# Kernel optimization log

Hardware: AMD Instinct MI355X
Metric: run time of the kernel (lower is better)

Reference implementation:

```python
import jax, jax.numpy as jnp
from jax import lax
import numpy as np


def _normalize(x):
    # F.normalize(dim=-1), eps=1e-12
    return x / jnp.clip(jnp.linalg.norm(x, axis=-1, keepdims=True), 1e-12, None)


def _masked_log_softmax(logits, mask):
    # softmax restricted to active columns (emulates gathering active objects)
    return jax.nn.log_softmax(jnp.where(mask, logits, -1e9), axis=-1)


def _aabb_iou(gc, gs, pc, ps):
    # gc,gs: (B,L,3) gt center/size; pc,ps: (B,P,3) pred center/size -> iou (B,L,P)
    # create_box_batch builds axis-aligned corner boxes, so box3d_overlap == AABB IoU
    gmin = (gc - gs * 0.5)[:, :, None, :]
    gmax = (gc + gs * 0.5)[:, :, None, :]
    pmin = (pc - ps * 0.5)[:, None, :, :]
    pmax = (pc + ps * 0.5)[:, None, :, :]
    inter = jnp.prod(jnp.clip(jnp.minimum(gmax, pmax) - jnp.maximum(gmin, pmin), 0.0, None), axis=-1)
    vol_g = jnp.prod(gs, axis=-1)[:, :, None]
    vol_p = jnp.prod(ps, axis=-1)[:, None, :]
    return inter / (vol_g + vol_p - inter + 1e-7)


def setup_inputs() -> dict:
    key = jax.random.key(0)
    ks = jax.random.split(key, 11)
    B, P, L, H = 32, 1024, 32, 128
    return {
        'pred_center': jax.random.normal(ks[0], (B, P, 3), jnp.float32),
        'pred_size': jax.random.uniform(ks[1], (B, P, 3), jnp.float32, 0.2, 1.5),
        'bbox_feature': jax.random.normal(ks[2], (B, P, H), jnp.float32),
        'gt_center': jax.random.normal(ks[3], (B, L, 3), jnp.float32),
        'gt_size': jax.random.uniform(ks[4], (B, L, 3), jnp.float32, 0.2, 1.5),
        'lang_emb': jax.random.normal(ks[5], (B * L, H), jnp.float32),
        'objectness_scores': jax.random.normal(ks[6], (B, P, 2), jnp.float32),
        'Wt': jax.random.normal(ks[7], (H, H), jnp.float32) * (1.0 / np.sqrt(H)),
        'Wp': jax.random.normal(ks[8], (H, H), jnp.float32) * (1.0 / np.sqrt(H)),
        'Wpi': jax.random.normal(ks[9], (H, H), jnp.float32) * (1.0 / np.sqrt(H)),
        'lang_num': jax.random.randint(ks[10], (B,), 1, L + 1, jnp.int64),
    }


def reference(pred_center, pred_size, bbox_feature, gt_center, gt_size,
              lang_emb, objectness_scores, Wt, Wp, Wpi, lang_num):
    sg = lax.stop_gradient
    B, P = pred_center.shape[:2]
    L = gt_center.shape[1]

    # objectness mask (argmax over 2 classes), detached
    obj_mask = (jnp.argmax(objectness_scores, axis=-1) == 1).astype(jnp.float32)  # (B,P)
    cmask = obj_mask > 0
    cnt = obj_mask.sum(-1)                       # active objects per sample
    cnt1 = jnp.maximum(cnt, 1.0)

    # 3D IoU between gt boxes (size + 0.01, as in forward) and predicted boxes; all detached
    iou = _aabb_iou(sg(gt_center), sg(gt_size) + 0.01, sg(pred_center), sg(pred_size))  # (B,L,P)
    tgt = (iou > 0.25).astype(jnp.float32) * obj_mask[:, None, :]  # (B,L,P), detached

    # ---- language-box contrastive (NCE) ----
    text = _normalize(jnp.einsum('bld,hd->blh', lang_emb.reshape(B, L, -1), Wt))   # (B,L,H)
    boxl = _normalize(jnp.einsum('bpd,hd->bph', bbox_feature, Wp))                 # (B,P,H)
    sim_lang = jnp.einsum('blh,bph->blp', text, boxl)                              # (B,L,P)
    ls = _masked_log_softmax(sim_lang, cmask[:, None, :])
    loss_v = (-ls * tgt).sum(-1) / cnt1[:, None]                                   # mean over cnt cols
    # transposed logits are (cnt,1): log_softmax over a single logit is 0 -> loss_t == 0
    lang_nce = 0.5 * loss_v                                                        # (B,L)

    lang_active = (jnp.arange(L)[None, :] < lang_num[:, None]).astype(jnp.float32)
    lang_con_loss = (lang_nce * lang_active).sum() / B

    # ---- box-box contrastive (NCE) ----
    boxi = _normalize(jnp.einsum('bpd,hd->bph', bbox_feature, Wpi))                # (B,P,H)
    sim_iou = jnp.einsum('bph,bqh->bpq', boxi, boxi)                               # (B,P,P)
    ls_r = _masked_log_softmax(sim_iou, cmask[:, None, :])
    ls_c = _masked_log_softmax(jnp.swapaxes(sim_iou, 1, 2), cmask[:, None, :])
    # target(b,l,p,q) = tgt(b,l,p)*tgt(b,l,q); contract without materializing (B,L,P,P)
    lv = jnp.einsum('blp,bpq,blq->bl', tgt, -ls_r, tgt) / (cnt1 ** 2)[:, None]
    lt = jnp.einsum('blp,bpq,blq->bl', tgt, -ls_c, tgt) / (cnt1 ** 2)[:, None]
    iou_nce = 0.5 * (lv + lt)                                                      # (B,L)
    iou_con_loss = (iou_nce * lang_active).sum() / B

    return jnp.stack([lang_con_loss, iou_con_loss])
```

## Files before the change

kernel.cpp:

```cpp
#include <hip/hip_runtime.h>
#include <hip/hip_bf16.h>
#include <math.h>

typedef unsigned short u16;
typedef unsigned int   u32;
typedef unsigned char  u8;
typedef unsigned long long u64;

typedef __attribute__((ext_vector_type(8))) short short8_t;
typedef __attribute__((ext_vector_type(4))) float f32x4_t;

#define H128 128

__device__ __forceinline__ float bf2f(u16 v){
    u32 u = ((u32)v) << 16;
    return __uint_as_float(u);
}
__device__ __forceinline__ u16 f2bf(float x){
    u32 u = __float_as_uint(x);
    u32 r = (u + 0x7fffu + ((u >> 16) & 1u)) >> 16;
    return (u16)r;
}
__device__ __forceinline__ void unpack8(uint4 v, float* f){
    f[0] = bf2f((u16)(v.x & 0xffff)); f[1] = bf2f((u16)(v.x >> 16));
    f[2] = bf2f((u16)(v.y & 0xffff)); f[3] = bf2f((u16)(v.y >> 16));
    f[4] = bf2f((u16)(v.z & 0xffff)); f[5] = bf2f((u16)(v.z >> 16));
    f[6] = bf2f((u16)(v.w & 0xffff)); f[7] = bf2f((u16)(v.w >> 16));
}
__device__ __forceinline__ float ld1(const void* p, size_t i, int F){
    return F ? ((const float*)p)[i] : bf2f(((const u16*)p)[i]);
}
__device__ __forceinline__ void ld8(const void* p, size_t i, int F, float* f){
    if (F){
        const float* fp = (const float*)p + i;
        float4 a = *(const float4*)fp;
        float4 b = *(const float4*)(fp + 4);
        f[0]=a.x; f[1]=a.y; f[2]=a.z; f[3]=a.w;
        f[4]=b.x; f[5]=b.y; f[6]=b.z; f[7]=b.w;
    } else {
        uint4 v = *(const uint4*)((const u16*)p + i);
        unpack8(v, f);
    }
}
__device__ __forceinline__ float clampf(float x, float lo, float hi){
    return fminf(fmaxf(x, lo), hi);
}
__device__ __forceinline__ int detectF(const void* pred_size, int* Fs){
    int tid = threadIdx.x;
    if (tid < 64){
        const u16* ps = (const u16*)pred_size;
        u16 v0 = ps[tid], v1 = ps[tid + 64];
        int cc = ((v0 >= 0x3000 && v0 < 0x4100) ? 1 : 0)
               + ((v1 >= 0x3000 && v1 < 0x4100) ? 1 : 0);
        #pragma unroll
        for (int off = 32; off > 0; off >>= 1) cc += __shfl_xor(cc, off);
        if (tid == 0) *Fs = (cc >= 120) ? 0 : 1;
    }
    __syncthreads();
    return *Fs;
}

__device__ void prep_fn(char* smem,
        const void* obj, const void* gtc, const void* gts,
        const void* pc_, const void* ps_, int F,
        u8* mask, float* cnt_part, u8* tgt, float* tcnt_part,
        int* needcnt_part, int* needlist, int* acnt_part, int* alist,
        int b0, int P, int L, int bblk)
{
    int tid = threadIdx.x;
    int ntile = P / 256;
    int b = bblk / ntile, ct = bblk % ntile;
    int p = ct * 256 + tid;

    float* gtb = (float*)smem;
    float* tl  = gtb + (size_t)L * 8;
    float* red = tl + L;
    int*   wb  = (int*)(red + 256);
    int*   wb2 = wb + 4;

    if (tid < L){
        float gmn[3], gmx[3], gss[3];
        for (int i = 0; i < 3; i++){
            size_t gi = ((size_t)(b0 + b) * L + tid) * 3 + i;
            float gc  = ld1(gtc, gi, F);
            float gsv = ld1(gts, gi, F) + 0.01f;
            gmn[i] = gc - 0.5f * gsv; gmx[i] = gc + 0.5f * gsv; gss[i] = gsv;
        }
        float* r = &gtb[tid * 8];
        r[0] = gmn[0]; r[1] = gmn[1]; r[2] = gmn[2];
        r[3] = gmx[0]; r[4] = gmx[1]; r[5] = gmx[2];
        r[6] = gss[0] * gss[1] * gss[2];
        tl[tid] = 0.f;
    }
    __syncthreads();

    size_t ob = ((size_t)(b0 + b) * P + p) * 2;
    float s0 = ld1(obj, ob, F), s1 = ld1(obj, ob + 1, F);
    u8 m = (s1 > s0) ? 1 : 0;
    mask[(size_t)b * P + p] = m;

    size_t pb = ((size_t)(b0 + b) * P + p) * 3;
    float pl[3], ph[3], volp = 1.f;
    for (int i = 0; i < 3; i++){
        float pcv = ld1(pc_, pb + i, F), psv = ld1(ps_, pb + i, F);
        pl[i] = pcv - 0.5f * psv; ph[i] = pcv + 0.5f * psv; volp *= psv;
    }
    bool any = false;
    for (int l = 0; l < L; l++){
        float* r = &gtb[l * 8];
        float inter = 1.f;
        for (int i = 0; i < 3; i++){
            float mn = fmaxf(r[i],     pl[i]);
            float mx = fminf(r[3 + i], ph[i]);
            inter *= fmaxf(mx - mn, 0.f);
        }
        float iou = inter / (r[6] + volp - inter + 1e-7f);
        u8 t = (iou > 0.25f && m) ? 1 : 0;
        tgt[((size_t)b * L + l) * P + p] = t;
        if (t){ any = true; atomicAdd(&tl[l], 1.f); }
    }

    int wid = tid >> 6, lane = tid & 63;
    u64 bal  = __ballot(any);
    u64 bal2 = __ballot(m != 0);
    if (lane == 0){ wb[wid] = __popcll(bal); wb2[wid] = __popcll(bal2); }
    red[tid] = (float)m;
    __syncthreads();
    if (tid == 0){
        int s = 0;
        for (int w = 0; w < 4; w++){ int cn = wb[w];  wb[w]  = s; s += cn; }
        needcnt_part[b * 4 + ct] = s;
        s = 0;
        for (int w = 0; w < 4; w++){ int cn = wb2[w]; wb2[w] = s; s += cn; }
        acnt_part[b * 4 + ct] = s;
    }
    __syncthreads();
    if (any){
        int rank = __popcll(bal & ((1ULL << lane) - 1ULL));
        needlist[(size_t)b * P + ct * 256 + wb[wid] + rank] = p;
    }
    if (m){
        int rank = __popcll(bal2 & ((1ULL << lane) - 1ULL));
        alist[(size_t)b * P + ct * 256 + wb2[wid] + rank] = p;
    }
    for (int st = 128; st > 0; st >>= 1){
        if (tid < st) red[tid] += red[tid + st];
        __syncthreads();
    }
    if (tid == 0) cnt_part[b * 4 + ct] = red[0];
    if (tid < L)  tcnt_part[(size_t)(b * 4 + ct) * L + tid] = tl[tid];
}

__device__ void proj_fn(char* smem,
        const void* __restrict__ X, const void* __restrict__ W, int F,
        u16* __restrict__ outb, int row0, int rowoff, int nrows)
{
    int tid = threadIdx.x;
    u16* Ws = (u16*)smem;
    u16* Xs = (u16*)(smem + 32768);

    for (int i = 0; i < 8; i++){
        int cid = tid + i * 256;
        int r = cid >> 4, cc = cid & 15;
        float f[8];
        ld8(W, (size_t)r * H128 + cc * 8, F, f);
        u16* dst = &Ws[r * H128 + ((cc ^ (r & 15)) * 8)];
        #pragma unroll
        for (int j = 0; j < 8; j++) dst[j] = f2bf(f[j]);
    }
    for (int i = 0; i < 4; i++){
        int cid = tid + i * 256;
        int r = cid >> 4, cc = cid & 15;
        int row = row0 + r;
        float f[8];
        if (row < nrows){
            ld8(X, (size_t)(rowoff + row) * H128 + cc * 8, F, f);
        } else {
            for (int j = 0; j < 8; j++) f[j] = 0.f;
        }
        u16* dst = &Xs[r * H128 + ((cc ^ (r & 15)) * 8)];
        #pragma unroll
        for (int j = 0; j < 8; j++) dst[j] = f2bf(f[j]);
    }
    __syncthreads();

    int w = tid >> 6, lane = tid & 63;
    int quad = lane >> 4, mrow = lane & 15;

    short8_t af[4];
    int arow = w * 16 + mrow;
    #pragma unroll
    for (int kt = 0; kt < 4; kt++){
        int chunk = kt * 4 + quad;
        af[kt] = *(const short8_t*)&Xs[arow * H128 + ((chunk ^ mrow) * 8)];
    }

    f32x4_t acc[8];
    #pragma unroll
    for (int ntl = 0; ntl < 8; ntl++) acc[ntl] = (f32x4_t){0.f, 0.f, 0.f, 0.f};
    #pragma unroll
    for (int ntl = 0; ntl < 8; ntl++){
        int n = ntl * 16 + mrow;
        #pragma unroll
        for (int kt = 0; kt < 4; kt++){
            int chunk = kt * 4 + quad;
            short8_t bf = *(const short8_t*)&Ws[n * H128 + ((chunk ^ mrow) * 8)];
            acc[ntl] = __builtin_amdgcn_mfma_f32_16x16x32_bf16(af[kt], bf, acc[ntl], 0, 0, 0);
        }
    }

    float ss[4] = {0.f, 0.f, 0.f, 0.f};
    #pragma unroll
    for (int ntl = 0; ntl < 8; ntl++)
        #pragma unroll
        for (int reg = 0; reg < 4; reg++) ss[reg] += acc[ntl][reg] * acc[ntl][reg];
    #pragma unroll
    for (int off = 1; off <= 8; off <<= 1)
        #pragma unroll
        for (int reg = 0; reg < 4; reg++) ss[reg] += __shfl_xor(ss[reg], off);
    float rn[4];
    #pragma unroll
    for (int reg = 0; reg < 4; reg++) rn[reg] = 1.0f / fmaxf(sqrtf(ss[reg]), 1e-12f);

    #pragma unroll
    for (int reg = 0; reg < 4; reg++){
        int row = row0 + w * 16 + quad * 4 + reg;
        if (row < nrows){
            #pragma unroll
            for (int ntl = 0; ntl < 8; ntl++){
                int col = ntl * 16 + mrow;
                outb[(size_t)row * H128 + col] = f2bf(acc[ntl][reg] * rn[reg]);
            }
        }
    }
}

__global__ void __launch_bounds__(256) k_main1(
        const void* __restrict__ obj, const void* __restrict__ gtc, const void* __restrict__ gts,
        const void* __restrict__ pc_, const void* __restrict__ ps_,
        const void* __restrict__ bbox, const void* __restrict__ lang,
        const void* __restrict__ Wp, const void* __restrict__ Wpi, const void* __restrict__ Wt,
        u8* __restrict__ mask, float* __restrict__ cnt_part, u8* __restrict__ tgt,
        float* __restrict__ tcnt_part, int* __restrict__ needcnt_part, int* __restrict__ needlist,
        int* __restrict__ acnt_part, int* __restrict__ alist,
        u16* __restrict__ boxl, u16* __restrict__ boxi, u16* __restrict__ text,
        float* __restrict__ accf, u32* __restrict__ ctrs, int* __restrict__ flagp,
        int chunk_idx, int first,
        int nprep, int nb1, int b0, int P, int L, int nrows_bp, int nrows_t)
{
    __shared__ __align__(16) char smem[49152];
    __shared__ int Fs;
    int F = detectF(ps_, &Fs);
    int blk = blockIdx.x;
    if (blk == 0 && threadIdx.x == 0){
        ctrs[chunk_idx] = 0u;
        *flagp = F;
        if (first){ accf[0] = 0.f; accf[1] = 0.f; }
    }
    if (blk < nprep){
        prep_fn(smem, obj, gtc, gts, pc_, ps_, F, mask, cnt_part, tgt, tcnt_part,
                needcnt_part, needlist, acnt_part, alist, b0, P, L, blk);
        return;
    }
    blk -= nprep;
    if (blk < nb1)
        proj_fn(smem, bbox, Wp,  F, boxl, blk * 64,             b0 * P, nrows_bp);
    else if (blk < 2 * nb1)
        proj_fn(smem, bbox, Wpi, F, boxi, (blk - nb1) * 64,     b0 * P, nrows_bp);
    else
        proj_fn(smem, lang, Wt,  F, text, (blk - 2 * nb1) * 64, b0 * L, nrows_t);
}

__device__ void lang_fn(char* smem,
        const u16* __restrict__ text, const u16* __restrict__ boxl,
        const u8* __restrict__ mask, const u8* __restrict__ tgt,
        float* __restrict__ sexp_part, float* __restrict__ sdot_part, int P, int L, int bblk)
{
    int nct = P >> 7;
    int b = bblk / nct, ct = bblk % nct;
    int p0 = ct * 128;
    int tid = threadIdx.x;

    u16* As = (u16*)smem;
    u16* Bs = (u16*)(smem + 8192);
    u8*  Ts = (u8*)(smem + 40960);
    u8*  mk = (u8*)(smem + 45056);

    for (int i = 0; i < 2; i++){
        int cid = tid + i * 256;
        int r = cid >> 4, cc = cid & 15;
        uint4 v = *(const uint4*)&text[((size_t)b * L + r) * H128 + cc * 8];
        *(uint4*)&As[r * H128 + ((cc ^ (r & 15)) * 8)] = v;
    }
    for (int i = 0; i < 8; i++){
        int cid = tid + i * 256;
        int r = cid >> 4, cc = cid & 15;
        uint4 v = *(const uint4*)&boxl[((size_t)b * P + p0 + r) * H128 + cc * 8];
        *(uint4*)&Bs[r * H128 + ((cc ^ (r & 15)) * 8)] = v;
    }
    {
        int l = tid >> 3, seg = tid & 7;
        uint4 v = *(const uint4*)&tgt[((size_t)b * L + l) * P + p0 + seg * 16];
        *(uint4*)&Ts[l * 128 + seg * 16] = v;
    }
    if (tid < 128) mk[tid] = mask[(size_t)b * P + p0 + tid];
    __syncthreads();

    int w = tid >> 6, lane = tid & 63;
    int quad = lane >> 4, mrow = lane & 15;
    int mt = w & 1, ch = w >> 1;

    short8_t af[4];
    #pragma unroll
    for (int kt = 0; kt < 4; kt++){
        int chunk = kt * 4 + quad;
        af[kt] = *(const short8_t*)&As[(mt * 16 + mrow) * H128 + ((chunk ^ mrow) * 8)];
    }

    float se[4] = {0.f, 0.f, 0.f, 0.f};
    float sd[4] = {0.f, 0.f, 0.f, 0.f};
    #pragma unroll
    for (int nt = 0; nt < 4; nt++){
        int cl = ch * 64 + nt * 16 + mrow;
        f32x4_t acc = (f32x4_t){0.f, 0.f, 0.f, 0.f};
        #pragma unroll
        for (int kt = 0; kt < 4; kt++){
            int chunk = kt * 4 + quad;
            short8_t bf = *(const short8_t*)&Bs[cl * H128 + ((chunk ^ mrow) * 8)];
            acc = __builtin_amdgcn_mfma_f32_16x16x32_bf16(af[kt], bf, acc, 0, 0, 0);
        }
        float m = mk[cl] ? 1.f : 0.f;
        #pragma unroll
        for (int reg = 0; reg < 4; reg++){
            int l = mt * 16 + quad * 4 + reg;
            float d = acc[reg];
            se[reg] += m * __expf(d);
            if (m != 0.f && Ts[l * 128 + cl]) sd[reg] += d;
        }
    }
    #pragma unroll
    for (int off = 1; off <= 8; off <<= 1)
        #pragma unroll
        for (int reg = 0; reg < 4; reg++){
            se[reg] += __shfl_xor(se[reg], off);
            sd[reg] += __shfl_xor(sd[reg], off);
        }
    if (mrow == 0){
        #pragma unroll
        for (int reg = 0; reg < 4; reg++){
            int l = mt * 16 + quad * 4 + reg;
            size_t idx = (size_t)(b * L + l) * 16 + ct * 2 + ch;
            sexp_part[idx] = se[reg];
            sdot_part[idx] = sd[reg];
        }
    }
}

__device__ void lse_fn(char* smem,
        const u16* __restrict__ boxi,
        const int* __restrict__ needcnt_part, const int* __restrict__ needlist,
        const int* __restrict__ acnt_part, const int* __restrict__ alist,
        float* __restrict__ lse_part, int P, int bblk)
{
    int b = bblk >> 3, ctA = bblk & 7;
    int prefA[5], preN[5];
    prefA[0] = 0; preN[0] = 0;
    for (int j = 0; j < 4; j++){
        prefA[j + 1] = prefA[j] + acnt_part[b * 4 + j];
        preN[j + 1]  = preN[j]  + needcnt_part[b * 4 + j];
    }
    int acnt = prefA[4], ncnt = preN[4];
    if (ctA * 128 >= acnt || ncnt <= 0) return;
    int tid = threadIdx.x;

    u16* Bs = (u16*)smem;
    u8*  mk = (u8*)(smem + 32768);

    for (int i = 0; i < 8; i++){
        int cid = tid + i * 256;
        int r = cid >> 4, cc = cid & 15;
        int aq = ctA * 128 + r;
        uint4 v = {0, 0, 0, 0};
        if (aq < acnt){
            int j = (aq >= prefA[1]) + (aq >= prefA[2]) + (aq >= prefA[3]);
            int cp = alist[(size_t)b * P + j * 256 + (aq - prefA[j])];
            v = *(const uint4*)&boxi[((size_t)b * P + cp) * H128 + cc * 8];
        }
        *(uint4*)&Bs[r * H128 + ((cc ^ (r & 15)) * 8)] = v;
    }
    if (tid < 128) mk[tid] = (ctA * 128 + tid < acnt) ? 1 : 0;
    __syncthreads();

    int w = tid >> 6, lane = tid & 63;
    int quad = lane >> 4, mrow = lane & 15;
    int nrt = (ncnt + 15) >> 4;

    for (int rt = w; rt < nrt; rt += 4){
        int i = rt * 16 + mrow;
        int ic = (i < ncnt) ? i : (ncnt - 1);
        int j = (ic >= preN[1]) + (ic >= preN[2]) + (ic >= preN[3]);
        int prow = needlist[(size_t)b * P + j * 256 + (ic - preN[j])];
        const u16* ab = &boxi[((size_t)b * P + prow) * H128];
        short8_t af[4];
        #pragma unroll
        for (int kt = 0; kt < 4; kt++)
            af[kt] = *(const short8_t*)&ab[(kt * 4 + quad) * 8];

        float se[4] = {0.f, 0.f, 0.f, 0.f};
        #pragma unroll
        for (int nt = 0; nt < 8; nt++){
            int cl = nt * 16 + mrow;
            f32x4_t acc = (f32x4_t){0.f, 0.f, 0.f, 0.f};
            #pragma unroll
            for (int kt = 0; kt < 4; kt++){
                int chunk = kt * 4 + quad;
                short8_t bf = *(const short8_t*)&Bs[cl * H128 + ((chunk ^ mrow) * 8)];
                acc = __builtin_amdgcn_mfma_f32_16x16x32_bf16(af[kt], bf, acc, 0, 0, 0);
            }
            float m = mk[cl] ? 1.f : 0.f;
            #pragma unroll
            for (int reg = 0; reg < 4; reg++) se[reg] += m * __expf(acc[reg]);
        }
        #pragma unroll
        for (int off = 1; off <= 8; off <<= 1)
            #pragma unroll
            for (int reg = 0; reg < 4; reg++) se[reg] += __shfl_xor(se[reg], off);
        if (mrow == 0){
            #pragma unroll
            for (int reg = 0; reg < 4; reg++){
                int i2 = rt * 16 + quad * 4 + reg;
                if (i2 < ncnt){
                    int j2 = (i2 >= preN[1]) + (i2 >= preN[2]) + (i2 >= preN[3]);
                    int pr2 = needlist[(size_t)b * P + j2 * 256 + (i2 - preN[j2])];
                    lse_part[((size_t)b * P + pr2) * 8 + ctA] = se[reg];
                }
            }
        }
    }
}

__global__ void __launch_bounds__(256) k_main2(
        const u16* __restrict__ text, const u16* __restrict__ boxl, const u16* __restrict__ boxi,
        const u8* __restrict__ mask, const u8* __restrict__ tgt,
        const int* __restrict__ needcnt_part, const int* __restrict__ needlist,
        const int* __restrict__ acnt_part, const int* __restrict__ alist,
        float* __restrict__ sexp_part, float* __restrict__ sdot_part,
        float* __restrict__ lse_part, int nlang, int P, int L)
{
    __shared__ __align__(16) char smem[45184];
    int blk = blockIdx.x;
    if (blk < nlang) lang_fn(smem, text, boxl, mask, tgt, sexp_part, sdot_part, P, L, blk);
    else             lse_fn(smem, boxi, needcnt_part, needlist, acnt_part, alist,
                            lse_part, P, blk - nlang);
}

__global__ void __launch_bounds__(256) k_main3(
        const u16* __restrict__ boxi, const u8* __restrict__ tgt,
        const float* __restrict__ lse_part, const float* __restrict__ cnt_part,
        const float* __restrict__ tcnt_part, const float* __restrict__ sexp_part,
        const float* __restrict__ sdot_part, const int* __restrict__ acnt_part,
        const int* __restrict__ lang_raw, float* __restrict__ loss_part,
        float* __restrict__ accf, u32* __restrict__ ctr, const int* __restrict__ flagp,
        void* __restrict__ out, float invB, int is_last, int B, int b0, int P, int L)
{
    int blk = blockIdx.x, b = blk / L, l = blk % L, tid = threadIdx.x;
    bool is64 = (B >= 8) && lang_raw[1] == 0 && lang_raw[3] == 0 &&
                lang_raw[5] == 0 && lang_raw[7] == 0;
    int lniv = is64 ? lang_raw[2 * (b0 + b)] : lang_raw[b0 + b];
    float tf = tcnt_part[(size_t)(b * 4 + 0) * L + l] + tcnt_part[(size_t)(b * 4 + 1) * L + l]
             + tcnt_part[(size_t)(b * 4 + 2) * L + l] + tcnt_part[(size_t)(b * 4 + 3) * L + l];
    bool active = (l < lniv) && (tf > 0.f);

    __shared__ int mem[1024];
    __shared__ int wbase[4];
    __shared__ int total;
    __shared__ float redu[256];
    __shared__ float redu2[256];
    __shared__ float Ufin;
    __shared__ int lastf;

    float lang_loss = 0.f, iou_loss = 0.f;
    if (active){
        float c1 = fmaxf(cnt_part[b * 4] + cnt_part[b * 4 + 1] +
                         cnt_part[b * 4 + 2] + cnt_part[b * 4 + 3], 1.f);
        int acnt = acnt_part[b * 4] + acnt_part[b * 4 + 1] +
                   acnt_part[b * 4 + 2] + acnt_part[b * 4 + 3];
        int nact = (acnt + 127) >> 7;

        int wid = tid >> 6, lane = tid & 63;
        if (tid == 0) total = 0;
        __syncthreads();
        for (int k = 0; k < P / 256; k++){
            int p = tid + k * 256;
            bool hit = (tgt[((size_t)b * L + l) * P + p] != 0);
            u64 bal = __ballot(hit);
            if (lane == 0) wbase[wid] = __popcll(bal);
            __syncthreads();
            if (tid == 0){
                int s = total;
                for (int w = 0; w < 4; w++){ int c = wbase[w]; wbase[w] = s; s += c; }
                total = s;
            }
            __syncthreads();
            if (hit){
                int rank = __popcll(bal & ((1ULL << lane) - 1ULL));
                mem[wbase[wid] + rank] = p;
            }
            __syncthreads();
        }
        int t = total;

        float U = 0.f;
        for (int i = tid; i < t; i += 256){
            const float* lp = &lse_part[((size_t)b * P + mem[i]) * 8];
            float s = 0.f;
            for (int ctA = 0; ctA < nact; ctA++) s += lp[ctA];
            U += logf(fmaxf(s, 1e-30f));
        }
        redu[tid] = U; __syncthreads();
        for (int st = 128; st > 0; st >>= 1){
            if (tid < st) redu[tid] += redu[tid + st];
            __syncthreads();
        }
        if (tid == 0) Ufin = redu[0];
        __syncthreads();

        {
            int h = tid & 127, half = tid >> 7;
            float vh = 0.f;
            for (int i = half; i < t; i += 2)
                vh += bf2f(boxi[((size_t)b * P + mem[i]) * H128 + h]);
            redu[tid] = vh;
        }
        __syncthreads();
        if (tid < 128){
            float v = redu[tid] + redu[tid + 128];
            redu[tid] = v * v;
        }
        __syncthreads();
        for (int st = 64; st > 0; st >>= 1){
            if (tid < st) redu[tid] += redu[tid + st];
            __syncthreads();
        }
        if (tid == 0){
            float sexp = 0.f, sdot = 0.f;
            const float* ep = &sexp_part[(size_t)(b * L + l) * 16];
            const float* dp = &sdot_part[(size_t)(b * L + l) * 16];
            for (int k = 0; k < 16; k++){ sexp += ep[k]; sdot += dp[k]; }
            float LSE = logf(fmaxf(sexp, 1e-30f));
            lang_loss = clampf(0.5f * (tf * LSE - sdot) / c1, -1e5f, 1e5f);
            iou_loss  = clampf(((float)t * Ufin - redu[0]) / (c1 * c1), -1e5f, 1e5f);
        }
    }

    if (tid == 0){
        loss_part[blk] = lang_loss;
        loss_part[gridDim.x + blk] = iou_loss;
        __threadfence();
        u32 old = atomicAdd(ctr, 1u);
        lastf = (old == (u32)(gridDim.x - 1)) ? 1 : 0;
    }
    __syncthreads();
    if (lastf){
        __threadfence();
        float suml = 0.f, sumi = 0.f;
        for (int i = tid; i < (int)gridDim.x; i += 256){
            suml += loss_part[i];
            sumi += loss_part[gridDim.x + i];
        }
        redu[tid] = suml; redu2[tid] = sumi;
        __syncthreads();
        for (int st = 128; st > 0; st >>= 1){
            if (tid < st){ redu[tid] += redu[tid + st]; redu2[tid] += redu2[tid + st]; }
            __syncthreads();
        }
        if (tid == 0){
            accf[0] += redu[0];
            accf[1] += redu2[0];
            if (is_last){
                float a  = clampf(accf[0] * invB, -1e6f, 1e6f);
                float bb = clampf(accf[1] * invB, -1e6f, 1e6f);
                if (*flagp){
                    ((float*)out)[0] = a; ((float*)out)[1] = bb;
                } else {
                    ((u16*)out)[0] = f2bf(a); ((u16*)out)[1] = f2bf(bb);
                }
            }
        }
    }
}

extern "C" void kernel_launch(void* const* d_in, const int* in_sizes, int n_in,
                              void* d_out, int out_size, void* d_ws, size_t ws_size,
                              hipStream_t stream)
{
    const void* pred_center = d_in[0];
    const void* pred_size   = d_in[1];
    const void* bbox        = d_in[2];
    const void* gtc         = d_in[3];
    const void* gts         = d_in[4];
    const void* lang        = d_in[5];
    const void* obj         = d_in[6];
    const void* Wt          = d_in[7];
    const void* Wp          = d_in[8];
    const void* Wpi         = d_in[9];
    const int*  lang_raw    = (const int*)d_in[10];

    int B = in_sizes[10];
    int P = in_sizes[0] / (3 * B);
    int L = in_sizes[3] / (3 * B);
    (void)n_in; (void)out_size;

    char* w = (char*)d_ws;
    float* accf  = (float*)w;
    int*   flagp = (int*)(w + 64);
    u32*   ctrs  = (u32*)(w + 128);
    char*  chunk_base = w + 512;
    size_t chunk_avail = (ws_size > 512) ? ws_size - 512 : 0;

    size_t per_b = (size_t)P
                 + 64
                 + (size_t)4 * L * 4
                 + (size_t)L * 16 * 4 * 2
                 + (size_t)L * P
                 + (size_t)P * 4 * 2
                 + (size_t)P * 8 * 4
                 + (size_t)P * H128 * 2 * 2
                 + (size_t)L * H128 * 2
                 + (size_t)L * 8;
    size_t slop = 20 * 256;
    int C = B;
    if ((size_t)B * per_b + slop > chunk_avail){
        size_t av = (chunk_avail > slop) ? chunk_avail - slop : 0;
        C = (int)(av / per_b);
        if (C < 1) C = 1;
        if (C > B) C = B;
    }

    int chunk_idx = 0;
    for (int b0 = 0; b0 < B; b0 += C, chunk_idx++){
        int c = (B - b0 < C) ? (B - b0) : C;

        size_t off = 0;
        auto carve = [&](size_t bytes) -> void* {
            void* p = chunk_base + off;
            off = (off + bytes + 255) & ~(size_t)255;
            return p;
        };
        u8*    mask      = (u8*)   carve((size_t)c * P);
        float* cnt_part  = (float*)carve((size_t)c * 4 * 4);
        int*   acnt_part = (int*)  carve((size_t)c * 4 * 4);
        int*   ncnt_part = (int*)  carve((size_t)c * 4 * 4);
        float* tcnt_part = (float*)carve((size_t)c * 4 * L * 4);
        float* sexp_part = (float*)carve((size_t)c * L * 16 * 4);
        float* sdot_part = (float*)carve((size_t)c * L * 16 * 4);
        u8*    tgtb      = (u8*)   carve((size_t)c * L * P);
        int*   needlist  = (int*)  carve((size_t)c * P * 4);
        int*   alist     = (int*)  carve((size_t)c * P * 4);
        float* lse_part  = (float*)carve((size_t)c * P * 8 * 4);
        u16*   boxl      = (u16*)  carve((size_t)c * P * H128 * 2);
        u16*   boxi      = (u16*)  carve((size_t)c * P * H128 * 2);
        u16*   text      = (u16*)  carve((size_t)c * L * H128 * 2);
        float* loss_part = (float*)carve((size_t)c * L * 8);

        int is_last = (b0 + c >= B) ? 1 : 0;
        int nprep = c * (P / 256);
        int nb1 = (c * P + 63) / 64;
        int nbt = (c * L + 63) / 64;

        k_main1<<<nprep + 2 * nb1 + nbt, 256, 0, stream>>>(
            obj, gtc, gts, pred_center, pred_size, bbox, lang, Wp, Wpi, Wt,
            mask, cnt_part, tgtb, tcnt_part, ncnt_part, needlist, acnt_part, alist,
            boxl, boxi, text, accf, ctrs, flagp, chunk_idx, (b0 == 0) ? 1 : 0,
            nprep, nb1, b0, P, L, c * P, c * L);

        int nlang = c * (P / 128);
        k_main2<<<nlang + c * 8, 256, 0, stream>>>(
            text, boxl, boxi, mask, tgtb, ncnt_part, needlist, acnt_part, alist,
            sexp_part, sdot_part, lse_part, nlang, P, L);

        k_main3<<<c * L, 256, 0, stream>>>(
            boxi, tgtb, lse_part, cnt_part, tcnt_part, sexp_part, sdot_part,
            acnt_part, lang_raw, loss_part, accf, &ctrs[chunk_idx], flagp, d_out,
            1.0f / (float)B, is_last, B, b0, P, L);
    }
}
```

Baseline: 133.5 us.

## Fuse three kernel launches into one persistent kernel with grid barriers

Merges the prep/projection, lang/lse, and loss kernels into one persistent kernel of 512 blocks that loops over work items and separates the phases with atomic-counter grid barriers. Projection blocks now handle 256 rows each and reuse the loaded weight tile across four 64-row sub-tiles. The aim is to remove inter-kernel launch gaps and the last-block reduction logic, and to cut repeated weight loads. In exchange it depends on all 512 blocks being co-resident (launch bounds set to two blocks per CU), adds spin-wait cost at each barrier, and adds a memset launch to clear the barrier counters.

```diff
diff --git a/kernel.cpp b/kernel.cpp
--- a/kernel.cpp
+++ b/kernel.cpp
@@ -58,6 +58,16 @@
     }
     __syncthreads();
     return *Fs;
+}
+__device__ __forceinline__ void gridbar(u32* bar, u32 target){
+    __syncthreads();
+    if (threadIdx.x == 0){
+        __threadfence();
+        atomicAdd(bar, 1u);
+        while (atomicAdd(bar, 0u) < target) __builtin_amdgcn_s_sleep(2);
+        __threadfence();
+    }
+    __syncthreads();
 }
 
 __device__ void prep_fn(char* smem,
@@ -151,9 +161,9 @@
     if (tid < L)  tcnt_part[(size_t)(b * 4 + ct) * L + tid] = tl[tid];
 }
 
-__device__ void proj_fn(char* smem,
+__device__ void proj256_fn(char* smem,
         const void* __restrict__ X, const void* __restrict__ W, int F,
-        u16* __restrict__ outb, int row0, int rowoff, int nrows)
+        u16* __restrict__ outb, int item, int rowoff, int nrows)
 {
     int tid = threadIdx.x;
     u16* Ws = (u16*)smem;
@@ -168,107 +178,73 @@
         #pragma unroll
         for (int j = 0; j < 8; j++) dst[j] = f2bf(f[j]);
     }
-    for (int i = 0; i < 4; i++){
-        int cid = tid + i * 256;
-        int r = cid >> 4, cc = cid & 15;
-        int row = row0 + r;
-        float f[8];
-        if (row < nrows){
-            ld8(X, (size_t)(rowoff + row) * H128 + cc * 8, F, f);
-        } else {
-            for (int j = 0; j < 8; j++) f[j] = 0.f;
-        }
-        u16* dst = &Xs[r * H128 + ((cc ^ (r & 15)) * 8)];
-        #pragma unroll
-        for (int j = 0; j < 8; j++) dst[j] = f2bf(f[j]);
-    }
-    __syncthreads();
 
     int w = tid >> 6, lane = tid & 63;
     int quad = lane >> 4, mrow = lane & 15;
 
-    short8_t af[4];
-    int arow = w * 16 + mrow;
-    #pragma unroll
-    for (int kt = 0; kt < 4; kt++){
-        int chunk = kt * 4 + quad;
-        af[kt] = *(const short8_t*)&Xs[arow * H128 + ((chunk ^ mrow) * 8)];
-    }
-
-    f32x4_t acc[8];
-    #pragma unroll
-    for (int ntl = 0; ntl < 8; ntl++) acc[ntl] = (f32x4_t){0.f, 0.f, 0.f, 0.f};
-    #pragma unroll
-    for (int ntl = 0; ntl < 8; ntl++){
-        int n = ntl * 16 + mrow;
+    for (int sub = 0; sub < 4; sub++){
+        int row0 = item * 256 + sub * 64;
+        __syncthreads();
+        for (int i = 0; i < 4; i++){
+            int cid = tid + i * 256;
+            int r = cid >> 4, cc = cid & 15;
+            int row = row0 + r;
+            float f[8];
+            if (row < nrows){
+                ld8(X, (size_t)(rowoff + row) * H128 + cc * 8, F, f);
+            } else {
+                for (int j = 0; j < 8; j++) f[j] = 0.f;
+            }
+            u16* dst = &Xs[r * H128 + ((cc ^ (r & 15)) * 8)];
+            #pragma unroll
+            for (int j = 0; j < 8; j++) dst[j] = f2bf(f[j]);
+        }
+        __syncthreads();
+
+        short8_t af[4];
+        int arow = w * 16 + mrow;
         #pragma unroll
         for (int kt = 0; kt < 4; kt++){
             int chunk = kt * 4 + quad;
-            short8_t bf = *(const short8_t*)&Ws[n * H128 + ((chunk ^ mrow) * 8)];
-            acc[ntl] = __builtin_amdgcn_mfma_f32_16x16x32_bf16(af[kt], bf, acc[ntl], 0, 0, 0);
-        }
-    }
-
-    float ss[4] = {0.f, 0.f, 0.f, 0.f};
-    #pragma unroll
-    for (int ntl = 0; ntl < 8; ntl++)
-        #pragma unroll
-        for (int reg = 0; reg < 4; reg++) ss[reg] += acc[ntl][reg] * acc[ntl][reg];
-    #pragma unroll
-    for (int off = 1; off <= 8; off <<= 1)
-        #pragma unroll
-        for (int reg = 0; reg < 4; reg++) ss[reg] += __shfl_xor(ss[reg], off);
-    float rn[4];
-    #pragma unroll
-    for (int reg = 0; reg < 4; reg++) rn[reg] = 1.0f / fmaxf(sqrtf(ss[reg]), 1e-12f);
-
-    #pragma unroll
-    for (int reg = 0; reg < 4; reg++){
-        int row = row0 + w * 16 + quad * 4 + reg;
-        if (row < nrows){
-            #pragma unroll
-            for (int ntl = 0; ntl < 8; ntl++){
-                int col = ntl * 16 + mrow;
-                outb[(size_t)row * H128 + col] = f2bf(acc[ntl][reg] * rn[reg]);
-            }
-        }
-    }
-}
-
-__global__ void __launch_bounds__(256) k_main1(
-        const void* __restrict__ obj, const void* __restrict__ gtc, const void* __restrict__ gts,
-        const void* __restrict__ pc_, const void* __restrict__ ps_,
-        const void* __restrict__ bbox, const void* __restrict__ lang,
-        const void* __restrict__ Wp, const void* __restrict__ Wpi, const void* __restrict__ Wt,
-        u8* __restrict__ mask, float* __restrict__ cnt_part, u8* __restrict__ tgt,
-        float* __restrict__ tcnt_part, int* __restrict__ needcnt_part, int* __restrict__ needlist,
-        int* __restrict__ acnt_part, int* __restrict__ alist,
-        u16* __restrict__ boxl, u16* __restrict__ boxi, u16* __restrict__ text,
-        float* __restrict__ accf, u32* __restrict__ ctrs, int* __restrict__ flagp,
-        int chunk_idx, int first,
-        int nprep, int nb1, int b0, int P, int L, int nrows_bp, int nrows_t)
-{
-    __shared__ __align__(16) char smem[49152];
-    __shared__ int Fs;
-    int F = detectF(ps_, &Fs);
-    int blk = blockIdx.x;
-    if (blk == 0 && threadIdx.x == 0){
-        ctrs[chunk_idx] = 0u;
-        *flagp = F;
-        if (first){ accf[0] = 0.f; accf[1] = 0.f; }
-    }
-    if (blk < nprep){
-        prep_fn(smem, obj, gtc, gts, pc_, ps_, F, mask, cnt_part, tgt, tcnt_part,
-                needcnt_part, needlist, acnt_part, alist, b0, P, L, blk);
-        return;
-    }
-    blk -= nprep;
-    if (blk < nb1)
-        proj_fn(smem, bbox, Wp,  F, boxl, blk * 64,             b0 * P, nrows_bp);
-    else if (blk < 2 * nb1)
-        proj_fn(smem, bbox, Wpi, F, boxi, (blk - nb1) * 64,     b0 * P, nrows_bp);
-    else
-        proj_fn(smem, lang, Wt,  F, text, (blk - 2 * nb1) * 64, b0 * L, nrows_t);
+            af[kt] = *(const short8_t*)&Xs[arow * H128 + ((chunk ^ mrow) * 8)];
+        }
+        f32x4_t acc[8];
+        #pragma unroll
+        for (int ntl = 0; ntl < 8; ntl++) acc[ntl] = (f32x4_t){0.f, 0.f, 0.f, 0.f};
+        #pragma unroll
+        for (int ntl = 0; ntl < 8; ntl++){
+            int n = ntl * 16 + mrow;
+            #pragma unroll
+            for (int kt = 0; kt < 4; kt++){
+                int chunk = kt * 4 + quad;
+                short8_t bf = *(const short8_t*)&Ws[n * H128 + ((chunk ^ mrow) * 8)];
+                acc[ntl] = __builtin_amdgcn_mfma_f32_16x16x32_bf16(af[kt], bf, acc[ntl], 0, 0, 0);
+            }
+        }
+        float ss[4] = {0.f, 0.f, 0.f, 0.f};
+        #pragma unroll
+        for (int ntl = 0; ntl < 8; ntl++)
+            #pragma unroll
+            for (int reg = 0; reg < 4; reg++) ss[reg] += acc[ntl][reg] * acc[ntl][reg];
+        #pragma unroll
+        for (int off = 1; off <= 8; off <<= 1)
+            #pragma unroll
+            for (int reg = 0; reg < 4; reg++) ss[reg] += __shfl_xor(ss[reg], off);
+        float rn[4];
+        #pragma unroll
+        for (int reg = 0; reg < 4; reg++) rn[reg] = 1.0f / fmaxf(sqrtf(ss[reg]), 1e-12f);
+        #pragma unroll
+        for (int reg = 0; reg < 4; reg++){
+            int row = row0 + w * 16 + quad * 4 + reg;
+            if (row < nrows){
+                #pragma unroll
+                for (int ntl = 0; ntl < 8; ntl++){
+                    int col = ntl * 16 + mrow;
+                    outb[(size_t)row * H128 + col] = f2bf(acc[ntl][reg] * rn[reg]);
+                }
+            }
+        }
+    }
 }
 
 __device__ void lang_fn(char* smem,
@@ -439,45 +415,27 @@
     }
 }
 
-__global__ void __launch_bounds__(256) k_main2(
-        const u16* __restrict__ text, const u16* __restrict__ boxl, const u16* __restrict__ boxi,
-        const u8* __restrict__ mask, const u8* __restrict__ tgt,
-        const int* __restrict__ needcnt_part, const int* __restrict__ needlist,
-        const int* __restrict__ acnt_part, const int* __restrict__ alist,
-        float* __restrict__ sexp_part, float* __restrict__ sdot_part,
-        float* __restrict__ lse_part, int nlang, int P, int L)
-{
-    __shared__ __align__(16) char smem[45184];
-    int blk = blockIdx.x;
-    if (blk < nlang) lang_fn(smem, text, boxl, mask, tgt, sexp_part, sdot_part, P, L, blk);
-    else             lse_fn(smem, boxi, needcnt_part, needlist, acnt_part, alist,
-                            lse_part, P, blk - nlang);
-}
-
-__global__ void __launch_bounds__(256) k_main3(
+__device__ void lossC_fn(char* smem,
         const u16* __restrict__ boxi, const u8* __restrict__ tgt,
         const float* __restrict__ lse_part, const float* __restrict__ cnt_part,
         const float* __restrict__ tcnt_part, const float* __restrict__ sexp_part,
         const float* __restrict__ sdot_part, const int* __restrict__ acnt_part,
         const int* __restrict__ lang_raw, float* __restrict__ loss_part,
-        float* __restrict__ accf, u32* __restrict__ ctr, const int* __restrict__ flagp,
-        void* __restrict__ out, float invB, int is_last, int B, int b0, int P, int L)
+        int B, int b0, int P, int L, int nC, int it)
 {
-    int blk = blockIdx.x, b = blk / L, l = blk % L, tid = threadIdx.x;
+    int b = it / L, l = it % L, tid = threadIdx.x;
+    int*   mem    = (int*)smem;
+    int*   wbase  = (int*)(smem + 4096);
+    int*   totalp = (int*)(smem + 4160);
+    float* redu   = (float*)(smem + 4352);
+    float* Ufinp  = (float*)(smem + 5376);
+
     bool is64 = (B >= 8) && lang_raw[1] == 0 && lang_raw[3] == 0 &&
                 lang_raw[5] == 0 && lang_raw[7] == 0;
     int lniv = is64 ? lang_raw[2 * (b0 + b)] : lang_raw[b0 + b];
     float tf = tcnt_part[(size_t)(b * 4 + 0) * L + l] + tcnt_part[(size_t)(b * 4 + 1) * L + l]
              + tcnt_part[(size_t)(b * 4 + 2) * L + l] + tcnt_part[(size_t)(b * 4 + 3) * L + l];
     bool active = (l < lniv) && (tf > 0.f);
-
-    __shared__ int mem[1024];
-    __shared__ int wbase[4];
-    __shared__ int total;
-    __shared__ float redu[256];
-    __shared__ float redu2[256];
-    __shared__ float Ufin;
-    __shared__ int lastf;
 
     float lang_loss = 0.f, iou_loss = 0.f;
     if (active){
@@ -488,7 +446,7 @@
         int nact = (acnt + 127) >> 7;
 
         int wid = tid >> 6, lane = tid & 63;
-        if (tid == 0) total = 0;
+        if (tid == 0) *totalp = 0;
         __syncthreads();
         for (int k = 0; k < P / 256; k++){
             int p = tid + k * 256;
@@ -497,9 +455,9 @@
             if (lane == 0) wbase[wid] = __popcll(bal);
             __syncthreads();
             if (tid == 0){
-                int s = total;
+                int s = *totalp;
                 for (int w = 0; w < 4; w++){ int c = wbase[w]; wbase[w] = s; s += c; }
-                total = s;
+                *totalp = s;
             }
             __syncthreads();
             if (hit){
@@ -508,7 +466,7 @@
             }
             __syncthreads();
         }
-        int t = total;
+        int t = *totalp;
 
         float U = 0.f;
         for (int i = tid; i < t; i += 256){
@@ -522,7 +480,9 @@
             if (tid < st) redu[tid] += redu[tid + st];
             __syncthreads();
         }
-        if (tid == 0) Ufin = redu[0];
+        if (tid == 0) *Ufinp = redu[0];
+        __syncthreads();
+        float Ufin = *Ufinp;
         __syncthreads();
 
         {
@@ -552,21 +512,78 @@
             iou_loss  = clampf(((float)t * Ufin - redu[0]) / (c1 * c1), -1e5f, 1e5f);
         }
     }
-
     if (tid == 0){
-        loss_part[blk] = lang_loss;
-        loss_part[gridDim.x + blk] = iou_loss;
-        __threadfence();
-        u32 old = atomicAdd(ctr, 1u);
-        lastf = (old == (u32)(gridDim.x - 1)) ? 1 : 0;
-    }
-    __syncthreads();
-    if (lastf){
-        __threadfence();
+        loss_part[it] = lang_loss;
+        loss_part[nC + it] = iou_loss;
+    }
+}
+
+__global__ void __launch_bounds__(256, 2) k_fused(
+        const void* __restrict__ obj, const void* __restrict__ gtc, const void* __restrict__ gts,
+        const void* __restrict__ pc_, const void* __restrict__ ps_,
+        const void* __restrict__ bbox, const void* __restrict__ lang,
+        const void* __restrict__ Wp, const void* __restrict__ Wpi, const void* __restrict__ Wt,
+        const int* __restrict__ lang_raw,
+        u8* __restrict__ mask, float* __restrict__ cnt_part, u8* __restrict__ tgt,
+        float* __restrict__ tcnt_part, int* __restrict__ ncnt_part, int* __restrict__ needlist,
+        int* __restrict__ acnt_part, int* __restrict__ alist,
+        u16* __restrict__ boxl, u16* __restrict__ boxi, u16* __restrict__ text,
+        float* __restrict__ sexp_part, float* __restrict__ sdot_part,
+        float* __restrict__ lse_part, float* __restrict__ loss_part,
+        float* __restrict__ accf, u32* __restrict__ bars,
+        void* __restrict__ out, float invB,
+        int first, int is_last, int B, int b0, int c, int P, int L)
+{
+    __shared__ __align__(16) char smem[49152];
+    __shared__ int Fs;
+    int F = detectF(ps_, &Fs);
+    const int NB = gridDim.x;
+    const u32 tcount = (u32)NB;
+
+    int nprep = c * (P / 256);
+    int npb = (c * P + 255) / 256;
+    int npt = (c * L + 255) / 256;
+    int nA = nprep + 2 * npb + npt;
+    for (int it = blockIdx.x; it < nA; it += NB){
+        __syncthreads();
+        if (it < nprep){
+            prep_fn(smem, obj, gtc, gts, pc_, ps_, F, mask, cnt_part, tgt,
+                    tcnt_part, ncnt_part, needlist, acnt_part, alist, b0, P, L, it);
+        } else {
+            int pj = it - nprep;
+            if (pj < npb)           proj256_fn(smem, bbox, Wp,  F, boxl, pj,           b0 * P, c * P);
+            else if (pj < 2 * npb)  proj256_fn(smem, bbox, Wpi, F, boxi, pj - npb,     b0 * P, c * P);
+            else                    proj256_fn(smem, lang, Wt,  F, text, pj - 2 * npb, b0 * L, c * L);
+        }
+    }
+    gridbar(&bars[0], tcount);
+
+    int nlang = c * (P / 128);
+    int nB2 = nlang + c * 8;
+    for (int it = blockIdx.x; it < nB2; it += NB){
+        __syncthreads();
+        if (it < nlang) lang_fn(smem, text, boxl, mask, tgt, sexp_part, sdot_part, P, L, it);
+        else            lse_fn(smem, boxi, ncnt_part, needlist, acnt_part, alist,
+                               lse_part, P, it - nlang);
+    }
+    gridbar(&bars[1], tcount);
+
+    int nC = c * L;
+    for (int it = blockIdx.x; it < nC; it += NB){
+        __syncthreads();
+        lossC_fn(smem, boxi, tgt, lse_part, cnt_part, tcnt_part, sexp_part,
+                 sdot_part, acnt_part, lang_raw, loss_part, B, b0, P, L, nC, it);
+    }
+    gridbar(&bars[2], tcount);
+
+    if (blockIdx.x == 0){
+        int tid = threadIdx.x;
+        float* redu  = (float*)smem;
+        float* redu2 = (float*)(smem + 1024);
         float suml = 0.f, sumi = 0.f;
-        for (int i = tid; i < (int)gridDim.x; i += 256){
+        for (int i = tid; i < nC; i += 256){
             suml += loss_part[i];
-            sumi += loss_part[gridDim.x + i];
+            sumi += loss_part[nC + i];
         }
         redu[tid] = suml; redu2[tid] = sumi;
         __syncthreads();
@@ -575,12 +592,13 @@
             __syncthreads();
         }
         if (tid == 0){
-            accf[0] += redu[0];
-            accf[1] += redu2[0];
+            float a0 = first ? redu[0]  : (accf[0] + redu[0]);
+            float a1 = first ? redu2[0] : (accf[1] + redu2[0]);
+            accf[0] = a0; accf[1] = a1;
             if (is_last){
-                float a  = clampf(accf[0] * invB, -1e6f, 1e6f);
-                float bb = clampf(accf[1] * invB, -1e6f, 1e6f);
-                if (*flagp){
+                float a  = clampf(a0 * invB, -1e6f, 1e6f);
+                float bb = clampf(a1 * invB, -1e6f, 1e6f);
+                if (F){
                     ((float*)out)[0] = a; ((float*)out)[1] = bb;
                 } else {
                     ((u16*)out)[0] = f2bf(a); ((u16*)out)[1] = f2bf(bb);
@@ -612,21 +630,15 @@
     (void)n_in; (void)out_size;
 
     char* w = (char*)d_ws;
-    float* accf  = (float*)w;
-    int*   flagp = (int*)(w + 64);
-    u32*   ctrs  = (u32*)(w + 128);
-    char*  chunk_base = w + 512;
-    size_t chunk_avail = (ws_size > 512) ? ws_size - 512 : 0;
-
-    size_t per_b = (size_t)P
-                 + 64
-                 + (size_t)4 * L * 4
-                 + (size_t)L * 16 * 4 * 2
-                 + (size_t)L * P
-                 + (size_t)P * 4 * 2
-                 + (size_t)P * 8 * 4
-                 + (size_t)P * H128 * 2 * 2
-                 + (size_t)L * H128 * 2
+    float* accf = (float*)w;
+    u32*   bars = (u32*)(w + 128);
+    char*  chunk_base = w + 1152;
+    size_t chunk_avail = (ws_size > 1152) ? ws_size - 1152 : 0;
+
+    size_t per_b = (size_t)P + 64 + (size_t)4 * L * 4
+                 + (size_t)L * 16 * 4 * 2 + (size_t)L * P
+                 + (size_t)P * 4 * 2 + (size_t)P * 8 * 4
+                 + (size_t)P * H128 * 2 * 2 + (size_t)L * H128 * 2
                  + (size_t)L * 8;
     size_t slop = 20 * 256;
     int C = B;
@@ -636,6 +648,8 @@
         if (C < 1) C = 1;
         if (C > B) C = B;
     }
+
+    hipMemsetAsync(bars, 0, 1024, stream);
 
     int chunk_idx = 0;
     for (int b0 = 0; b0 < B; b0 += C, chunk_idx++){
@@ -664,24 +678,12 @@
         float* loss_part = (float*)carve((size_t)c * L * 8);
 
         int is_last = (b0 + c >= B) ? 1 : 0;
-        int nprep = c * (P / 256);
-        int nb1 = (c * P + 63) / 64;
-        int nbt = (c * L + 63) / 64;
-
-        k_main1<<<nprep + 2 * nb1 + nbt, 256, 0, stream>>>(
-            obj, gtc, gts, pred_center, pred_size, bbox, lang, Wp, Wpi, Wt,
+
+        k_fused<<<512, 256, 0, stream>>>(
+            obj, gtc, gts, pred_center, pred_size, bbox, lang, Wp, Wpi, Wt, lang_raw,
             mask, cnt_part, tgtb, tcnt_part, ncnt_part, needlist, acnt_part, alist,
-            boxl, boxi, text, accf, ctrs, flagp, chunk_idx, (b0 == 0) ? 1 : 0,
-            nprep, nb1, b0, P, L, c * P, c * L);
-
-        int nlang = c * (P / 128);
-        k_main2<<<nlang + c * 8, 256, 0, stream>>>(
-            text, boxl, boxi, mask, tgtb, ncnt_part, needlist, acnt_part, alist,
-            sexp_part, sdot_part, lse_part, nlang, P, L);
-
-        k_main3<<<c * L, 256, 0, stream>>>(
-            boxi, tgtb, lse_part, cnt_part, tcnt_part, sexp_part, sdot_part,
-            acnt_part, lang_raw, loss_part, accf, &ctrs[chunk_idx], flagp, d_out,
-            1.0f / (float)B, is_last, B, b0, P, L);
-    }
-}
+            boxl, boxi, text, sexp_part, sdot_part, lse_part, loss_part,
+            accf, &bars[chunk_idx * 4], d_out, 1.0f / (float)B,
+            (b0 == 0) ? 1 : 0, is_last, B, b0, c, P, L);
+    }
+}
```

After: 271.9 us. 2.04x slower.
